# Optimization experiments

Measured on AMD Instinct MI355X. Metric: run time of the kernel, lower is better.

## Reference

```python
import jax, jax.numpy as jnp
import numpy as np

B, S, D, H = 4, 2048, 1024, 16
HD = D // H  # head dim = 64


def setup_inputs() -> dict:
    key = jax.random.key(0)
    k1, k2, k3 = jax.random.split(key, 3)
    return {
        "hidden_states": jax.random.normal(k1, (B, S, D), dtype=jnp.float32),
        "w_attn": jax.random.normal(k2, (D, 3 * D), dtype=jnp.float32) * 0.02,
        "b_attn": jnp.zeros((3 * D,), dtype=jnp.float32),
        "w_proj": jax.random.normal(k3, (D, D), dtype=jnp.float32) * 0.02,
        "b_proj": jnp.zeros((D,), dtype=jnp.float32),
    }


def reference(hidden_states, w_attn, b_attn, w_proj, b_proj):
    b, s, d = hidden_states.shape
    # fused QKV projection (Conv1D == x @ W + b)
    qkv = hidden_states @ w_attn + b_attn  # [b, s, 3d]
    q, k, v = jnp.split(qkv, 3, axis=-1)

    def split_heads(x):  # [b, s, d] -> [b, h, s, hd]
        return x.reshape(b, s, H, HD).transpose(0, 2, 1, 3)

    q, k, v = split_heads(q), split_heads(k), split_heads(v)

    scores = jnp.einsum("bhqd,bhkd->bhqk", q, k)  # [b, h, s, s]
    causal = jnp.tril(jnp.ones((s, s), dtype=scores.dtype))
    # source masks before scaling: w*b + -1e5*(1-b), then / sqrt(head_dim)
    scores = scores * causal + (-100000.0) * (1.0 - causal)
    scores = scores / jnp.sqrt(jnp.asarray(HD, dtype=scores.dtype))

    attn = jax.nn.softmax(scores, axis=-1)  # attn dropout is identity (p=0)
    ctx = jnp.einsum("bhqk,bhkd->bhqd", attn, v)  # [b, h, s, hd]
    ctx = ctx.transpose(0, 2, 1, 3).reshape(b, s, d)  # merge heads
    out = ctx @ w_proj + b_proj  # resid dropout identity (p=0)
    return out
```

## Files before the change

kernel.cpp:

```cpp
#include <hip/hip_runtime.h>
#include <hip/hip_bf16.h>

#define BB 4
#define SS 2048
#define DD 1024
#define HH 16
#define HD 64
#define MM (BB * SS)
#define NQKV (3 * DD)

typedef __attribute__((ext_vector_type(8))) _Float16 half8;
typedef __attribute__((ext_vector_type(4))) float f32x4;

static __device__ __forceinline__ unsigned short f2h(float f) {
  _Float16 h = (_Float16)f;
  return __builtin_bit_cast(unsigned short, h);
}

static __device__ __forceinline__ void gload_lds16(const void* g, void* l) {
  __builtin_amdgcn_global_load_lds(
      (const __attribute__((address_space(1))) unsigned int*)g,
      (__attribute__((address_space(3))) unsigned int*)l, 16, 0, 0);
}

__global__ __launch_bounds__(256) void cvt_f16(const float* __restrict__ in,
                                               unsigned short* __restrict__ out,
                                               int n4) {
  int i = blockIdx.x * 256 + threadIdx.x;
  if (i < n4) {
    float4 v = ((const float4*)in)[i];
    ushort4 o;
    o.x = f2h(v.x); o.y = f2h(v.y); o.z = f2h(v.z); o.w = f2h(v.w);
    ((ushort4*)out)[i] = o;
  }
}

__global__ __launch_bounds__(256) void transpose_f16(
    const float* __restrict__ in, unsigned short* __restrict__ out, int K, int N) {
  __shared__ float tile[64][65];
  const int k0 = blockIdx.y * 64, n0 = blockIdx.x * 64;
  const int t = threadIdx.x;
#pragma unroll
  for (int i = 0; i < 16; ++i) {
    int idx = i * 256 + t;
    int r = idx >> 6, c = idx & 63;
    tile[r][c] = in[(size_t)(k0 + r) * N + n0 + c];
  }
  __syncthreads();
#pragma unroll
  for (int i = 0; i < 16; ++i) {
    int idx = i * 256 + t;
    int r = idx >> 6, c = idx & 63;
    out[(size_t)(n0 + r) * K + k0 + c] = f2h(tile[c][r]);
  }
}

template <int MODE>
__global__ __launch_bounds__(256) void gemm_f16(
    const unsigned short* __restrict__ A, const unsigned short* __restrict__ BT,
    const float* __restrict__ bias, unsigned short* __restrict__ Cq,
    unsigned short* __restrict__ vT, float* __restrict__ Cf, int M, int N, int K) {
  __shared__ __align__(16) unsigned short As[128 * 32];
  __shared__ __align__(16) unsigned short Bs[128 * 32];

  const int t = threadIdx.x;
  const int lane = t & 63;
  const int w = t >> 6;
  const int wr = w >> 1, wc = w & 1;
  const int bm = blockIdx.y * 128, bn = blockIdx.x * 128;

  f32x4 acc[4][4] = {};

  const int srow = (lane >> 2);
  const int sslot = (lane & 3);

  for (int k0 = 0; k0 < K; k0 += 32) {
    __syncthreads();
#pragma unroll
    for (int i = 0; i < 2; ++i) {
      int chunk = w * 2 + i;
      int row = chunk * 16 + srow;
      int cs = sslot ^ ((row >> 1) & 3);
      gload_lds16(A + (size_t)(bm + row) * K + k0 + cs * 8,
                  (char*)As + chunk * 1024);
      gload_lds16(BT + (size_t)(bn + row) * K + k0 + cs * 8,
                  (char*)Bs + chunk * 1024);
    }
    __syncthreads();

    half8 af[4], bf[4];
#pragma unroll
    for (int mb = 0; mb < 4; ++mb) {
      int row = wr * 64 + mb * 16 + (lane & 15);
      int cs = (lane >> 4) ^ ((row >> 1) & 3);
      af[mb] = *(const half8*)((const char*)As + row * 64 + cs * 16);
    }
#pragma unroll
    for (int nb = 0; nb < 4; ++nb) {
      int row = wc * 64 + nb * 16 + (lane & 15);
      int cs = (lane >> 4) ^ ((row >> 1) & 3);
      bf[nb] = *(const half8*)((const char*)Bs + row * 64 + cs * 16);
    }
#pragma unroll
    for (int mb = 0; mb < 4; ++mb)
#pragma unroll
      for (int nb = 0; nb < 4; ++nb)
        acc[mb][nb] = __builtin_amdgcn_mfma_f32_16x16x32_f16(
            af[mb], bf[nb], acc[mb][nb], 0, 0, 0);
  }

  const int g = lane >> 4;
#pragma unroll
  for (int mb = 0; mb < 4; ++mb) {
#pragma unroll
    for (int nb = 0; nb < 4; ++nb) {
      int m0 = bm + wr * 64 + mb * 16 + g * 4;
      int n = bn + wc * 64 + nb * 16 + (lane & 15);
      float bv = bias[n];
      if (MODE == 0) {
        if (n < 2 * DD) {
#pragma unroll
          for (int r = 0; r < 4; ++r)
            Cq[(size_t)(m0 + r) * NQKV + n] = f2h(acc[mb][nb][r] + bv);
        } else {
          int h = (n - 2 * DD) >> 6;
          int hd = n & 63;
          int b = m0 >> 11, s0 = m0 & 2047;
          ushort4 pk;
          unsigned short* pp = (unsigned short*)&pk;
#pragma unroll
          for (int r = 0; r < 4; ++r) pp[r] = f2h(acc[mb][nb][r] + bv);
          *(ushort4*)&vT[((size_t)((b * HH + h) * HD + hd)) * SS + s0] = pk;
        }
      } else {
#pragma unroll
        for (int r = 0; r < 4; ++r)
          Cf[(size_t)(m0 + r) * N + n] = acc[mb][nb][r] + bv;
      }
    }
  }
}

__global__ __launch_bounds__(256) void flash16(
    const unsigned short* __restrict__ qkv,
    const unsigned short* __restrict__ vT,
    unsigned short* __restrict__ ctx) {
  __shared__ __align__(16) unsigned short Kt[64 * 64];
  __shared__ __align__(16) unsigned short Vt[64 * 64];
  __shared__ __align__(16) unsigned short Ps[4][16 * 72];

  const int t = threadIdx.x, lane = t & 63, w = t >> 6;
  const int qblk = blockIdx.x, bh = blockIdx.y;
  const int b = bh >> 4, h = bh & 15;
  const int q0 = qblk * 64;
  const int q = lane & 15;
  const int g = lane >> 4;
  const int qrow = q0 + w * 16 + q;

  half8 qf[2];
  {
    const unsigned short* qp = qkv + (size_t)(b * SS + qrow) * NQKV + h * HD;
    qf[0] = *(const half8*)(qp + g * 8);
    qf[1] = *(const half8*)(qp + 32 + g * 8);
  }

  f32x4 oacc[4] = {};
  float m_run = -1e30f, l_run = 0.f;

  const unsigned short* kg = qkv + (size_t)b * SS * NQKV + DD + h * HD;
  const unsigned short* vg = vT + (size_t)(b * HH + h) * HD * SS;
  unsigned short* pw = &Ps[w][0];

  for (int kt = 0; kt <= qblk; ++kt) {
    const int k0 = kt * 64;
    __syncthreads();
#pragma unroll
    for (int i = 0; i < 2; ++i) {
      int chunk = w * 2 + i;
      int row = chunk * 8 + (lane >> 3);
      int cs = (lane & 7) ^ (row & 7);
      gload_lds16(kg + (size_t)(k0 + row) * NQKV + cs * 8,
                  (char*)Kt + chunk * 1024);
      gload_lds16(vg + (size_t)row * SS + k0 + cs * 8,
                  (char*)Vt + chunk * 1024);
    }
    __syncthreads();

    f32x4 sacc[4] = {};
#pragma unroll
    for (int ks = 0; ks < 2; ++ks) {
#pragma unroll
      for (int kb = 0; kb < 4; ++kb) {
        int row = kb * 16 + q;
        int cs = (g + 4 * ks) ^ (row & 7);
        half8 kf = *(const half8*)((const char*)Kt + row * 128 + cs * 16);
        sacc[kb] =
            __builtin_amdgcn_mfma_f32_16x16x32_f16(kf, qf[ks], sacc[kb], 0, 0, 0);
      }
    }

    const bool diag = (kt == qblk);
    float s[4][4];
    float pmax = -1e30f;
#pragma unroll
    for (int kb = 0; kb < 4; ++kb)
#pragma unroll
      for (int r = 0; r < 4; ++r) {
        float v = sacc[kb][r] * 0.125f;
        if (diag) {
          int kk = k0 + kb * 16 + g * 4 + r;
          if (kk > qrow) v = -12500.f;
        }
        s[kb][r] = v;
        pmax = fmaxf(pmax, v);
      }
    pmax = fmaxf(pmax, __shfl_xor(pmax, 16));
    pmax = fmaxf(pmax, __shfl_xor(pmax, 32));
    float mnew = fmaxf(m_run, pmax);
    float scale = __expf(m_run - mnew);
    float lsum = 0.f;
    ushort4 pk[4];
#pragma unroll
    for (int kb = 0; kb < 4; ++kb) {
      unsigned short* pp = (unsigned short*)&pk[kb];
#pragma unroll
      for (int r = 0; r < 4; ++r) {
        float p = __expf(s[kb][r] - mnew);
        lsum += p;
        pp[r] = f2h(p);
      }
    }
    lsum += __shfl_xor(lsum, 16);
    lsum += __shfl_xor(lsum, 32);
    l_run = l_run * scale + lsum;
    m_run = mnew;
#pragma unroll
    for (int hb = 0; hb < 4; ++hb) oacc[hb] *= scale;

#pragma unroll
    for (int kb = 0; kb < 4; ++kb)
      *(ushort4*)((char*)pw + q * 144 + kb * 32 + g * 8) = pk[kb];
    __syncthreads();

#pragma unroll
    for (int ks = 0; ks < 2; ++ks) {
      half8 pf = *(const half8*)((const char*)pw + q * 144 + (g + 4 * ks) * 16);
#pragma unroll
      for (int hb = 0; hb < 4; ++hb) {
        int row = hb * 16 + q;
        int cs = (g + 4 * ks) ^ (row & 7);
        half8 vf = *(const half8*)((const char*)Vt + row * 128 + cs * 16);
        oacc[hb] = __builtin_amdgcn_mfma_f32_16x16x32_f16(vf, pf, oacc[hb], 0, 0, 0);
      }
    }
  }

  float inv = 1.f / l_run;
  unsigned short* cp = ctx + (size_t)(b * SS + qrow) * DD + h * HD;
#pragma unroll
  for (int hb = 0; hb < 4; ++hb) {
    ushort4 pk;
    unsigned short* pp = (unsigned short*)&pk;
#pragma unroll
    for (int r = 0; r < 4; ++r) pp[r] = f2h(oacc[hb][r] * inv);
    *(ushort4*)(cp + hb * 16 + g * 4) = pk;
  }
}

extern "C" void kernel_launch(void* const* d_in, const int* in_sizes, int n_in,
                              void* d_out, int out_size, void* d_ws,
                              size_t ws_size, hipStream_t stream) {
  const float* x = (const float*)d_in[0];
  const float* w_attn = (const float*)d_in[1];
  const float* b_attn = (const float*)d_in[2];
  const float* w_proj = (const float*)d_in[3];
  const float* b_proj = (const float*)d_in[4];
  float* out = (float*)d_out;

  unsigned short* xB = (unsigned short*)d_ws;
  unsigned short* qkvB = xB + (size_t)MM * DD;
  unsigned short* vTb = qkvB + (size_t)MM * NQKV;
  unsigned short* ctxB = vTb + (size_t)BB * HH * HD * SS;
  unsigned short* wqkvT = ctxB + (size_t)MM * DD;
  unsigned short* wprojT = wqkvT + (size_t)NQKV * DD;

  cvt_f16<<<dim3(MM * DD / 4 / 256), 256, 0, stream>>>(x, xB, MM * DD / 4);
  transpose_f16<<<dim3(NQKV / 64, DD / 64), 256, 0, stream>>>(w_attn, wqkvT, DD, NQKV);
  transpose_f16<<<dim3(DD / 64, DD / 64), 256, 0, stream>>>(w_proj, wprojT, DD, DD);

  gemm_f16<0><<<dim3(NQKV / 128, MM / 128), 256, 0, stream>>>(
      xB, wqkvT, b_attn, qkvB, vTb, nullptr, MM, NQKV, DD);

  flash16<<<dim3(SS / 64, BB * HH), 256, 0, stream>>>(qkvB, vTb, ctxB);

  gemm_f16<1><<<dim3(DD / 128, MM / 128), 256, 0, stream>>>(
      ctxB, wprojT, b_proj, nullptr, nullptr, out, MM, DD, DD);
}
```

Before: 347.1 us.

## Pair causal q-blocks, double-buffer K/V, remap blocks to XCDs, lazy rescale

The attention kernel now gives each block one low and one mirrored high query tile (p and 31-p), so every block does the same amount of causal work. K/V tiles are double-buffered so the next tile loads while the current one is computed. Softmax rescaling is skipped unless the running max grows by more than a threshold, and the P scratch layout is swizzled. Both GEMMs and attention use 1D grids remapped so related tiles land on the same XCD, and MFMA sections get raised wave priority. This adds register pressure from two sets of accumulators, and the lazy rescale loosens numerical bounds slightly.

Measured after the change: 295.3 us. 14.9% less time.

```diff
diff --git a/kernel.cpp b/kernel.cpp
--- a/kernel.cpp
+++ b/kernel.cpp
@@ -59,7 +59,8 @@
 __global__ __launch_bounds__(256) void gemm_f16(
     const unsigned short* __restrict__ A, const unsigned short* __restrict__ BT,
     const float* __restrict__ bias, unsigned short* __restrict__ Cq,
-    unsigned short* __restrict__ vT, float* __restrict__ Cf, int M, int N, int K) {
+    unsigned short* __restrict__ vT, float* __restrict__ Cf, int M, int N, int K,
+    int nx) {
   __shared__ __align__(16) unsigned short As[128 * 32];
   __shared__ __align__(16) unsigned short Bs[128 * 32];
 
@@ -67,7 +68,11 @@
   const int lane = t & 63;
   const int w = t >> 6;
   const int wr = w >> 1, wc = w & 1;
-  const int bm = blockIdx.y * 128, bn = blockIdx.x * 128;
+
+  const int nwg = gridDim.x;
+  const int per = nwg >> 3;
+  const int logical = (blockIdx.x & 7) * per + (blockIdx.x >> 3);
+  const int bm = (logical / nx) * 128, bn = (logical % nx) * 128;
 
   f32x4 acc[4][4] = {};
 
@@ -101,12 +106,14 @@
       int cs = (lane >> 4) ^ ((row >> 1) & 3);
       bf[nb] = *(const half8*)((const char*)Bs + row * 64 + cs * 16);
     }
+    __builtin_amdgcn_s_setprio(1);
 #pragma unroll
     for (int mb = 0; mb < 4; ++mb)
 #pragma unroll
       for (int nb = 0; nb < 4; ++nb)
         acc[mb][nb] = __builtin_amdgcn_mfma_f32_16x16x32_f16(
             af[mb], bf[nb], acc[mb][nb], 0, 0, 0);
+    __builtin_amdgcn_s_setprio(0);
   }
 
   const int g = lane >> 4;
@@ -141,129 +148,169 @@
   }
 }
 
-__global__ __launch_bounds__(256) void flash16(
+__global__ __launch_bounds__(256, 4) void flash16(
     const unsigned short* __restrict__ qkv,
     const unsigned short* __restrict__ vT,
     unsigned short* __restrict__ ctx) {
-  __shared__ __align__(16) unsigned short Kt[64 * 64];
-  __shared__ __align__(16) unsigned short Vt[64 * 64];
-  __shared__ __align__(16) unsigned short Ps[4][16 * 72];
-
-  const int t = threadIdx.x, lane = t & 63, w = t >> 6;
-  const int qblk = blockIdx.x, bh = blockIdx.y;
+  __shared__ __align__(16) unsigned short Kt[2][64 * 64];
+  __shared__ __align__(16) unsigned short Vt[2][64 * 64];
+  __shared__ __align__(16) unsigned short Ps[4][16 * 64];
+
+  const int tid = threadIdx.x, lane = tid & 63, w = tid >> 6;
+  const int phys = blockIdx.x;
+  const int logical = (phys & 7) * 128 + (phys >> 3);
+  const int bh = logical >> 4;
+  const int p = logical & 15;
   const int b = bh >> 4, h = bh & 15;
-  const int q0 = qblk * 64;
-  const int q = lane & 15;
-  const int g = lane >> 4;
-  const int qrow = q0 + w * 16 + q;
-
-  half8 qf[2];
-  {
-    const unsigned short* qp = qkv + (size_t)(b * SS + qrow) * NQKV + h * HD;
-    qf[0] = *(const half8*)(qp + g * 8);
-    qf[1] = *(const half8*)(qp + 32 + g * 8);
-  }
-
-  f32x4 oacc[4] = {};
-  float m_run = -1e30f, l_run = 0.f;
+  const int qHiB = 31 - p;
+
+  const int q = lane & 15, g = lane >> 4;
+  const int qrowLo = p * 64 + w * 16 + q;
+  const int qrowHi = qHiB * 64 + w * 16 + q;
 
   const unsigned short* kg = qkv + (size_t)b * SS * NQKV + DD + h * HD;
   const unsigned short* vg = vT + (size_t)(b * HH + h) * HD * SS;
+
+  half8 qfLo[2], qfHi[2];
+  {
+    const unsigned short* qp = qkv + (size_t)(b * SS + qrowLo) * NQKV + h * HD;
+    qfLo[0] = *(const half8*)(qp + g * 8);
+    qfLo[1] = *(const half8*)(qp + 32 + g * 8);
+    const unsigned short* qp2 = qkv + (size_t)(b * SS + qrowHi) * NQKV + h * HD;
+    qfHi[0] = *(const half8*)(qp2 + g * 8);
+    qfHi[1] = *(const half8*)(qp2 + 32 + g * 8);
+  }
+
+  f32x4 oLo[4] = {}, oHi[4] = {};
+  float mLo = -1e30f, lLo = 0.f, mHi = -1e30f, lHi = 0.f;
+
   unsigned short* pw = &Ps[w][0];
-
-  for (int kt = 0; kt <= qblk; ++kt) {
-    const int k0 = kt * 64;
-    __syncthreads();
+  const int srow = lane >> 3, sslot = lane & 7;
+
+  auto STAGE = [&](int tt, int c) {
+    const int k0s = tt * 64;
 #pragma unroll
     for (int i = 0; i < 2; ++i) {
       int chunk = w * 2 + i;
-      int row = chunk * 8 + (lane >> 3);
-      int cs = (lane & 7) ^ (row & 7);
-      gload_lds16(kg + (size_t)(k0 + row) * NQKV + cs * 8,
-                  (char*)Kt + chunk * 1024);
-      gload_lds16(vg + (size_t)row * SS + k0 + cs * 8,
-                  (char*)Vt + chunk * 1024);
-    }
-    __syncthreads();
-
-    f32x4 sacc[4] = {};
-#pragma unroll
-    for (int ks = 0; ks < 2; ++ks) {
+      int row = chunk * 8 + srow;
+      int cs = sslot ^ (row & 7);
+      gload_lds16(kg + (size_t)(k0s + row) * NQKV + cs * 8,
+                  (char*)Kt[c] + chunk * 1024);
+      gload_lds16(vg + (size_t)row * SS + k0s + cs * 8,
+                  (char*)Vt[c] + chunk * 1024);
+    }
+  };
+
+  auto QBLOCK = [&](const half8 (&qf)[2], f32x4 (&oa)[4], float& m_run,
+                    float& l_run, int qrow, int k0, int cur, bool diag) {
+    f32x4 sa[4] = {};
+    __builtin_amdgcn_s_setprio(1);
+#pragma unroll
+    for (int ks = 0; ks < 2; ++ks)
 #pragma unroll
       for (int kb = 0; kb < 4; ++kb) {
         int row = kb * 16 + q;
         int cs = (g + 4 * ks) ^ (row & 7);
-        half8 kf = *(const half8*)((const char*)Kt + row * 128 + cs * 16);
-        sacc[kb] =
-            __builtin_amdgcn_mfma_f32_16x16x32_f16(kf, qf[ks], sacc[kb], 0, 0, 0);
-      }
-    }
-
-    const bool diag = (kt == qblk);
-    float s[4][4];
+        half8 kf = *(const half8*)((const char*)Kt[cur] + row * 128 + cs * 16);
+        sa[kb] =
+            __builtin_amdgcn_mfma_f32_16x16x32_f16(kf, qf[ks], sa[kb], 0, 0, 0);
+      }
+    __builtin_amdgcn_s_setprio(0);
+
     float pmax = -1e30f;
 #pragma unroll
     for (int kb = 0; kb < 4; ++kb)
 #pragma unroll
       for (int r = 0; r < 4; ++r) {
-        float v = sacc[kb][r] * 0.125f;
+        float v = sa[kb][r] * 0.125f;
         if (diag) {
           int kk = k0 + kb * 16 + g * 4 + r;
           if (kk > qrow) v = -12500.f;
         }
-        s[kb][r] = v;
+        sa[kb][r] = v;
         pmax = fmaxf(pmax, v);
       }
     pmax = fmaxf(pmax, __shfl_xor(pmax, 16));
     pmax = fmaxf(pmax, __shfl_xor(pmax, 32));
-    float mnew = fmaxf(m_run, pmax);
-    float scale = __expf(m_run - mnew);
+    if (!__all(pmax - m_run <= 8.0f)) {
+      float mnew = fmaxf(m_run, pmax);
+      float sc = __expf(m_run - mnew);
+      l_run *= sc;
+#pragma unroll
+      for (int hb = 0; hb < 4; ++hb) oa[hb] *= sc;
+      m_run = mnew;
+    }
     float lsum = 0.f;
-    ushort4 pk[4];
 #pragma unroll
     for (int kb = 0; kb < 4; ++kb) {
-      unsigned short* pp = (unsigned short*)&pk[kb];
+      ushort4 pk;
+      unsigned short* pp = (unsigned short*)&pk;
 #pragma unroll
       for (int r = 0; r < 4; ++r) {
-        float p = __expf(s[kb][r] - mnew);
-        lsum += p;
-        pp[r] = f2h(p);
-      }
+        float pv = __expf(sa[kb][r] - m_run);
+        lsum += pv;
+        pp[r] = f2h(pv);
+      }
+      int slot = (2 * kb + (g >> 1)) ^ (q & 7);
+      *(ushort4*)((char*)pw + q * 128 + slot * 16 + (g & 1) * 8) = pk;
     }
     lsum += __shfl_xor(lsum, 16);
     lsum += __shfl_xor(lsum, 32);
-    l_run = l_run * scale + lsum;
-    m_run = mnew;
-#pragma unroll
-    for (int hb = 0; hb < 4; ++hb) oacc[hb] *= scale;
-
-#pragma unroll
-    for (int kb = 0; kb < 4; ++kb)
-      *(ushort4*)((char*)pw + q * 144 + kb * 32 + g * 8) = pk[kb];
-    __syncthreads();
-
+    l_run += lsum;
+
+    __builtin_amdgcn_s_setprio(1);
 #pragma unroll
     for (int ks = 0; ks < 2; ++ks) {
-      half8 pf = *(const half8*)((const char*)pw + q * 144 + (g + 4 * ks) * 16);
+      int pslot = (g + 4 * ks) ^ (q & 7);
+      half8 pf = *(const half8*)((const char*)pw + q * 128 + pslot * 16);
 #pragma unroll
       for (int hb = 0; hb < 4; ++hb) {
         int row = hb * 16 + q;
         int cs = (g + 4 * ks) ^ (row & 7);
-        half8 vf = *(const half8*)((const char*)Vt + row * 128 + cs * 16);
-        oacc[hb] = __builtin_amdgcn_mfma_f32_16x16x32_f16(vf, pf, oacc[hb], 0, 0, 0);
-      }
-    }
-  }
-
-  float inv = 1.f / l_run;
-  unsigned short* cp = ctx + (size_t)(b * SS + qrow) * DD + h * HD;
-#pragma unroll
-  for (int hb = 0; hb < 4; ++hb) {
-    ushort4 pk;
-    unsigned short* pp = (unsigned short*)&pk;
-#pragma unroll
-    for (int r = 0; r < 4; ++r) pp[r] = f2h(oacc[hb][r] * inv);
-    *(ushort4*)(cp + hb * 16 + g * 4) = pk;
+        half8 vf = *(const half8*)((const char*)Vt[cur] + row * 128 + cs * 16);
+        oa[hb] =
+            __builtin_amdgcn_mfma_f32_16x16x32_f16(vf, pf, oa[hb], 0, 0, 0);
+      }
+    }
+    __builtin_amdgcn_s_setprio(0);
+  };
+
+  STAGE(0, 0);
+  __syncthreads();
+
+  const int nt = qHiB + 1;
+  for (int t = 0; t < nt; ++t) {
+    const int cur = t & 1;
+    if (t + 1 < nt) STAGE(t + 1, cur ^ 1);
+    const int k0 = t * 64;
+    if (t <= p) QBLOCK(qfLo, oLo, mLo, lLo, qrowLo, k0, cur, t == p);
+    QBLOCK(qfHi, oHi, mHi, lHi, qrowHi, k0, cur, t == qHiB);
+    __syncthreads();
+  }
+
+  {
+    float inv = 1.f / lLo;
+    unsigned short* cp = ctx + (size_t)(b * SS + qrowLo) * DD + h * HD;
+#pragma unroll
+    for (int hb = 0; hb < 4; ++hb) {
+      ushort4 pk;
+      unsigned short* pp = (unsigned short*)&pk;
+#pragma unroll
+      for (int r = 0; r < 4; ++r) pp[r] = f2h(oLo[hb][r] * inv);
+      *(ushort4*)(cp + hb * 16 + g * 4) = pk;
+    }
+  }
+  {
+    float inv = 1.f / lHi;
+    unsigned short* cp = ctx + (size_t)(b * SS + qrowHi) * DD + h * HD;
+#pragma unroll
+    for (int hb = 0; hb < 4; ++hb) {
+      ushort4 pk;
+      unsigned short* pp = (unsigned short*)&pk;
+#pragma unroll
+      for (int r = 0; r < 4; ++r) pp[r] = f2h(oHi[hb][r] * inv);
+      *(ushort4*)(cp + hb * 16 + g * 4) = pk;
+    }
   }
 }
 
@@ -285,14 +332,16 @@
   unsigned short* wprojT = wqkvT + (size_t)NQKV * DD;
 
   cvt_f16<<<dim3(MM * DD / 4 / 256), 256, 0, stream>>>(x, xB, MM * DD / 4);
-  transpose_f16<<<dim3(NQKV / 64, DD / 64), 256, 0, stream>>>(w_attn, wqkvT, DD, NQKV);
-  transpose_f16<<<dim3(DD / 64, DD / 64), 256, 0, stream>>>(w_proj, wprojT, DD, DD);
-
-  gemm_f16<0><<<dim3(NQKV / 128, MM / 128), 256, 0, stream>>>(
-      xB, wqkvT, b_attn, qkvB, vTb, nullptr, MM, NQKV, DD);
-
-  flash16<<<dim3(SS / 64, BB * HH), 256, 0, stream>>>(qkvB, vTb, ctxB);
-
-  gemm_f16<1><<<dim3(DD / 128, MM / 128), 256, 0, stream>>>(
-      ctxB, wprojT, b_proj, nullptr, nullptr, out, MM, DD, DD);
-}
+  transpose_f16<<<dim3(NQKV / 64, DD / 64), 256, 0, stream>>>(w_attn, wqkvT, DD,
+                                                              NQKV);
+  transpose_f16<<<dim3(DD / 64, DD / 64), 256, 0, stream>>>(w_proj, wprojT, DD,
+                                                            DD);
+
+  gemm_f16<0><<<dim3((NQKV / 128) * (MM / 128)), 256, 0, stream>>>(
+      xB, wqkvT, b_attn, qkvB, vTb, nullptr, MM, NQKV, DD, NQKV / 128);
+
+  flash16<<<dim3(1024), 256, 0, stream>>>(qkvB, vTb, ctxB);
+
+  gemm_f16<1><<<dim3((DD / 128) * (MM / 128)), 256, 0, stream>>>(
+      ctxB, wprojT, b_proj, nullptr, nullptr, out, MM, DD, DD, DD / 128);
+}
```
